# Performance work log

Hardware: AMD Instinct MI355X
Metric: run time of the kernel (lower is better)

Reference implementation:

```python
import jax, jax.numpy as jnp
import numpy as np

D = 512
H = 8
DV = D // H  # 64
NEG_INF = -1e30


def setup_inputs() -> dict:
    key = jax.random.key(0)
    ks = jax.random.split(key, 10)
    B, S = 4, 2048
    x = jax.random.normal(ks[0], (B, D, S), dtype=jnp.float32)
    mask = jnp.ones((B, S), dtype=jnp.float32)
    s = 1.0 / np.sqrt(D)
    sv = 1.0 / np.sqrt(D)
    # per-head Linear(d -> dv) weights stacked: [H, dv, d] (torch Linear layout W @ x)
    Wq = jax.random.uniform(ks[1], (H, DV, D), jnp.float32, -s, s)
    bq = jax.random.uniform(ks[2], (H, DV), jnp.float32, -s, s)
    Wk = jax.random.uniform(ks[3], (H, DV, D), jnp.float32, -s, s)
    bk = jax.random.uniform(ks[4], (H, DV), jnp.float32, -s, s)
    Wv = jax.random.uniform(ks[5], (H, DV, D), jnp.float32, -s, s)
    bv = jax.random.uniform(ks[6], (H, DV), jnp.float32, -s, s)
    W0 = jax.random.uniform(ks[7], (D, D), jnp.float32, -sv, sv)
    b0 = jax.random.uniform(ks[8], (D,), jnp.float32, -sv, sv)
    return {"x": x, "mask": mask, "Wq": Wq, "bq": bq, "Wk": Wk, "bk": bk,
            "Wv": Wv, "bv": bv, "W0": W0, "b0": b0}


def reference(x, mask, Wq, bq, Wk, bk, Wv, bv, W0, b0):
    # x: [B, d, S] -> xt: [B, S, d]
    xt = jnp.transpose(x, (0, 2, 1))
    # fused per-head projections: [B, H, S, dv]
    q = jnp.einsum('bsd,hed->bhse', xt, Wq) + bq[None, :, None, :]
    k = jnp.einsum('bsd,hed->bhse', xt, Wk) + bk[None, :, None, :]
    v = jnp.einsum('bsd,hed->bhse', xt, Wv) + bv[None, :, None, :]
    dv = q.shape[-1]
    scores = jnp.einsum('bhse,bhte->bhst', q, k) * (1.0 / np.sqrt(dv))
    # mask_logits (QANet style): keep where mask==1, else -1e30; mask over key dim
    h_mask = mask[:, None, None, :]  # [B,1,1,S]
    scores = scores * h_mask + (1.0 - h_mask) * NEG_INF
    p = jax.nn.softmax(scores, axis=-1)
    # zero out fully-masked query rows via v_mask on query dim
    p = p * mask[:, None, :, None]
    out = jnp.einsum('bhst,bhte->bhse', p, v)  # [B,H,S,dv]
    # concat heads along feature dim -> [B, S, d]
    B, _, S, _ = out.shape
    heads = jnp.transpose(out, (0, 2, 1, 3)).reshape(B, S, -1)
    y = heads @ W0.T + b0  # output projection
    return jnp.transpose(y, (0, 2, 1))  # [B, d, S]
```

## Files before the change

kernel.cpp:

```cpp
#include <hip/hip_runtime.h>

#define B_  4
#define D_  512
#define H_  8
#define DV_ 64
#define S_  2048
#define LOG2E 1.442695041f

typedef __bf16 bf16;
typedef bf16  bf16x8 __attribute__((ext_vector_type(8)));
typedef bf16  bf16x4 __attribute__((ext_vector_type(4)));
typedef float f32x4  __attribute__((ext_vector_type(4)));

#define MFMA(a, b, c) __builtin_amdgcn_mfma_f32_16x16x32_bf16((a), (b), (c), 0, 0, 0)

#define GLOAD_LDS(g, l)                                                     \
    __builtin_amdgcn_global_load_lds(                                       \
        (const __attribute__((address_space(1))) void*)(g),                 \
        (__attribute__((address_space(3))) void*)(l), 16, 0, 0)

__global__ __launch_bounds__(256) void prep(
    const float* __restrict__ x, const float* __restrict__ Wq,
    const float* __restrict__ Wk, const float* __restrict__ Wv,
    const float* __restrict__ W0, bf16* __restrict__ xb, bf16* __restrict__ Wb) {
    const int bid = blockIdx.x;
    if (bid < 4096) {
        __shared__ float tile[32][33];
        const int sblk = bid % 64;
        const int dblk = (bid / 64) % 16;
        const int b    = bid / 1024;
        const int d0 = dblk * 32, s0 = sblk * 32;
        const int tx = threadIdx.x & 31;
        const int ty = threadIdx.x >> 5;
        const float* xp = x + (size_t)b * D_ * S_;
#pragma unroll
        for (int i = 0; i < 32; i += 8)
            tile[ty + i][tx] = xp[(size_t)(d0 + ty + i) * S_ + s0 + tx];
        __syncthreads();
        bf16* xbp = xb + ((size_t)b * S_ + s0) * D_ + d0;
#pragma unroll
        for (int i = 0; i < 32; i += 8)
            xbp[(size_t)(ty + i) * D_ + tx] = (bf16)tile[tx][ty + i];
    } else {
        const int f0 = ((bid - 4096) * 256 + threadIdx.x) * 16;
        const int src = f0 >> 18;
        const int off = f0 & 262143;
        const float* W = (src == 0) ? Wq : (src == 1) ? Wk : (src == 2) ? Wv : W0;
        float4 v0 = *(const float4*)&W[off];
        float4 v1 = *(const float4*)&W[off + 4];
        float4 v2 = *(const float4*)&W[off + 8];
        float4 v3 = *(const float4*)&W[off + 12];
        bf16x8 h0 = {(bf16)v0.x, (bf16)v0.y, (bf16)v0.z, (bf16)v0.w,
                     (bf16)v1.x, (bf16)v1.y, (bf16)v1.z, (bf16)v1.w};
        bf16x8 h1 = {(bf16)v2.x, (bf16)v2.y, (bf16)v2.z, (bf16)v2.w,
                     (bf16)v3.x, (bf16)v3.y, (bf16)v3.z, (bf16)v3.w};
        *(bf16x8*)&Wb[f0]     = h0;
        *(bf16x8*)&Wb[f0 + 8] = h1;
    }
}

__global__ __launch_bounds__(256) void gemm_qkv(
    const bf16* __restrict__ A, const bf16* __restrict__ Wb,
    const float* __restrict__ bq, const float* __restrict__ bk,
    const float* __restrict__ bv,
    bf16* __restrict__ Q, bf16* __restrict__ K, bf16* __restrict__ Vt) {
    __shared__ union {
        struct { bf16 A[8192]; bf16 B[8192]; } s;
        bf16 T[128][132];
    } sm;

    const int tid = threadIdx.x;
    const int w = tid >> 6, lane = tid & 63;
    const int m16 = lane & 15, quad = lane >> 4;
    const int wr = w & 1, wc = w >> 1;

    const int nblk = blockIdx.x % 12;
    const int mblk = blockIdx.x / 12;
    const int m0 = mblk * 128, n0 = nblk * 128;

    f32x4 acc[4][4];
#pragma unroll
    for (int i = 0; i < 4; ++i)
#pragma unroll
        for (int j = 0; j < 4; ++j) acc[i][j] = (f32x4){0.f, 0.f, 0.f, 0.f};

    for (int k0 = 0; k0 < D_; k0 += 64) {
        __syncthreads();
#pragma unroll
        for (int i = 0; i < 4; ++i) {
            const int c  = w * 4 + i;
            const int mt = c >> 1, kk = c & 1;
            const int row = mt * 16 + m16;
            const int col = k0 + kk * 32 + quad * 8;
            GLOAD_LDS(&A[(size_t)(m0 + row) * D_ + col],  &sm.s.A[(c * 64 + lane) * 8]);
            GLOAD_LDS(&Wb[(size_t)(n0 + row) * D_ + col], &sm.s.B[(c * 64 + lane) * 8]);
        }
        __syncthreads();
#pragma unroll
        for (int kk = 0; kk < 2; ++kk) {
            bf16x8 af[4], bfv[4];
#pragma unroll
            for (int t = 0; t < 4; ++t) {
                af[t]  = *(const bf16x8*)&sm.s.A[(((wr * 4 + t) * 2 + kk) * 64 + lane) * 8];
                bfv[t] = *(const bf16x8*)&sm.s.B[(((wc * 4 + t) * 2 + kk) * 64 + lane) * 8];
            }
#pragma unroll
            for (int mt = 0; mt < 4; ++mt)
#pragma unroll
                for (int nt = 0; nt < 4; ++nt)
                    acc[mt][nt] = MFMA(af[mt], bfv[nt], acc[mt][nt]);
        }
    }

    const int proj = n0 >> 9;
    const float* bias = (proj == 0) ? bq : (proj == 1) ? bk : bv;

    if (proj == 2) {
#pragma unroll
        for (int mt = 0; mt < 4; ++mt)
#pragma unroll
            for (int nt = 0; nt < 4; ++nt) {
                const int nr = (n0 + wc * 64 + nt * 16 + m16) & 511;
                const int h = nr >> 6, e = nr & 63;
                const float bia = bias[nr];
                const int srow = m0 + wr * 64 + mt * 16 + quad * 4;
                const int b = srow >> 11, s = srow & 2047;
                const int s2 = (s & ~31) | (quad * 8 + (mt & 1) * 4);
                bf16x4 hv;
#pragma unroll
                for (int r = 0; r < 4; ++r) hv[r] = (bf16)(acc[mt][nt][r] + bia);
                *(bf16x4*)&Vt[(((size_t)b * H_ + h) * DV_ + e) * S_ + s2] = hv;
            }
    } else {
        __syncthreads();
#pragma unroll
        for (int mt = 0; mt < 4; ++mt)
#pragma unroll
            for (int nt = 0; nt < 4; ++nt) {
                const int nloc = wc * 64 + nt * 16 + m16;
                const float bia = bias[(n0 + nloc) & 511];
#pragma unroll
                for (int r = 0; r < 4; ++r)
                    sm.T[wr * 64 + mt * 16 + quad * 4 + r][nloc] =
                        (bf16)(acc[mt][nt][r] + bia);
            }
        __syncthreads();
        const int rloc = tid >> 1, cb = (tid & 1) * 64;
        const int M = m0 + rloc, b = M >> 11, s = M & 2047;
        const int nrb = (n0 + cb) & 511;
        const int h = nrb >> 6;
        bf16* dst = ((proj == 0) ? Q : K) + (((size_t)b * H_ + h) * S_ + s) * DV_;
#pragma unroll
        for (int u = 0; u < 8; ++u)
            *(bf16x8*)&dst[u * 8] = *(const bf16x8*)&sm.T[rloc][cb + u * 8];
    }
}

#define LOADK(DST, TW)                                                       \
    {                                                                        \
        _Pragma("unroll")                                                    \
        for (int tt = 0; tt < 2; ++tt)                                       \
            _Pragma("unroll")                                                \
            for (int kk = 0; kk < 2; ++kk)                                   \
                DST[tt][kk] = *(const bf16x8*)&Kp[                           \
                    (size_t)((TW) + tt * 16 + m16) * DV_ + kk * 32 + quad * 8]; \
    }

#define COMPUTE(TW, KF)                                                      \
    {                                                                        \
        const int tw_ = (TW);                                                \
        bf16x8 vfr[4];                                                       \
        _Pragma("unroll")                                                    \
        for (int mt = 0; mt < 4; ++mt)                                       \
            vfr[mt] = *(const bf16x8*)&Vp[(size_t)(mt * 16 + m16) * S_ +     \
                                          tw_ + quad * 8];                   \
        const f32x4 m2a = *(const f32x4*)&sm.Ms[tw_ + quad * 4];             \
        const f32x4 m2b = *(const f32x4*)&sm.Ms[tw_ + 16 + quad * 4];        \
        f32x4 sc[2][4];                                                      \
        _Pragma("unroll")                                                    \
        for (int tt = 0; tt < 2; ++tt)                                       \
            _Pragma("unroll")                                                \
            for (int qt = 0; qt < 4; ++qt)                                   \
                sc[tt][qt] = (f32x4){0.f, 0.f, 0.f, 0.f};                    \
        _Pragma("unroll")                                                    \
        for (int kk = 0; kk < 2; ++kk)                                       \
            _Pragma("unroll")                                                \
            for (int tt = 0; tt < 2; ++tt)                                   \
                _Pragma("unroll")                                            \
                for (int qt = 0; qt < 4; ++qt)                               \
                    sc[tt][qt] = MFMA(KF[tt][kk], qf[qt][kk], sc[tt][qt]);   \
        f32x4 ngA, ngB;                                                      \
        _Pragma("unroll")                                                    \
        for (int r = 0; r < 4; ++r) {                                        \
            ngA[r] = (m2a[r] - LOG2E) * 8e29f;                               \
            ngB[r] = (m2b[r] - LOG2E) * 8e29f;                               \
        }                                                                    \
        bf16x8 pf[4];                                                        \
        _Pragma("unroll")                                                    \
        for (int qt = 0; qt < 4; ++qt)                                       \
            _Pragma("unroll")                                                \
            for (int r = 0; r < 4; ++r) {                                    \
                pf[qt][r] = (bf16)__builtin_amdgcn_exp2f(                    \
                    __builtin_fmaf(sc[0][qt][r], m2a[r], ngA[r]));           \
                pf[qt][4 + r] = (bf16)__builtin_amdgcn_exp2f(                \
                    __builtin_fmaf(sc[1][qt][r], m2b[r], ngB[r]));           \
            }                                                                \
        _Pragma("unroll")                                                    \
        for (int mt = 0; mt < 4; ++mt)                                       \
            _Pragma("unroll")                                                \
            for (int qt = 0; qt < 4; ++qt)                                   \
                o[mt][qt] = MFMA(vfr[mt], pf[qt], o[mt][qt]);                \
        _Pragma("unroll")                                                    \
        for (int qt = 0; qt < 4; ++qt)                                       \
            lacc[qt] = MFMA(ones, pf[qt], lacc[qt]);                         \
    }

__global__ __launch_bounds__(256, 2) void flash_attn(
    const bf16* __restrict__ Q, const bf16* __restrict__ K, const bf16* __restrict__ Vt,
    const float* __restrict__ mask, bf16* __restrict__ heads) {
    __shared__ union {
        float Ms[2048];
        struct { float O[64][65]; float L[64]; } red;
    } sm;

    const int bid  = blockIdx.x;
    const int bidx = (bid & 7) * 128 + (bid >> 3);
    const int qblk = bidx & 31;
    const int h    = (bidx >> 5) & 7;
    const int b    = bidx >> 8;
    const int q0   = qblk * 64;

    const int tid = threadIdx.x;
    const int w = tid >> 6, lane = tid & 63;
    const int m16 = lane & 15, quad = lane >> 4;

    const bf16* Qp = Q  + ((size_t)b * H_ + h) * S_ * DV_;
    const bf16* Kp = K  + ((size_t)b * H_ + h) * S_ * DV_;
    const bf16* Vp = Vt + ((size_t)b * H_ + h) * DV_ * S_;
    const float* mp = mask + (size_t)b * S_;

#pragma unroll
    for (int p = 0; p < 2; ++p) {
        const float4 mv = *(const float4*)&mp[(p * 256 + tid) * 4];
        f32x4 t = {mv.x * LOG2E, mv.y * LOG2E, mv.z * LOG2E, mv.w * LOG2E};
        *(f32x4*)&sm.Ms[(p * 256 + tid) * 4] = t;
    }

    bf16x8 qf[4][2];
#pragma unroll
    for (int qt = 0; qt < 4; ++qt)
#pragma unroll
        for (int kk = 0; kk < 2; ++kk) {
            bf16x8 v = *(const bf16x8*)&Qp[(size_t)(q0 + qt * 16 + m16) * DV_ +
                                           kk * 32 + quad * 8];
#pragma unroll
            for (int i = 0; i < 8; ++i) v[i] = (bf16)((float)v[i] * 0.125f);
            qf[qt][kk] = v;
        }

    bf16x8 ones;
#pragma unroll
    for (int i = 0; i < 8; ++i) ones[i] = (bf16)1.0f;

    f32x4 o[4][4];
    f32x4 lacc[4];
#pragma unroll
    for (int mt = 0; mt < 4; ++mt)
#pragma unroll
        for (int qt = 0; qt < 4; ++qt) o[mt][qt] = (f32x4){0.f, 0.f, 0.f, 0.f};
#pragma unroll
    for (int qt = 0; qt < 4; ++qt) lacc[qt] = (f32x4){0.f, 0.f, 0.f, 0.f};

    bf16x8 kfA[2][2], kfB[2][2];
    LOADK(kfA, w * 32);
    __syncthreads();

    for (int i = 0; i < 16; i += 2) {
        LOADK(kfB, (i + 1) * 128 + w * 32);
        COMPUTE(i * 128 + w * 32, kfA);
        if (i < 14) LOADK(kfA, (i + 2) * 128 + w * 32);
        COMPUTE((i + 1) * 128 + w * 32, kfB);
    }

    __syncthreads();
#pragma unroll
    for (int ww = 0; ww < 4; ++ww) {
        if (w == ww) {
#pragma unroll
            for (int mt = 0; mt < 4; ++mt)
#pragma unroll
                for (int qt = 0; qt < 4; ++qt)
#pragma unroll
                    for (int r = 0; r < 4; ++r) {
                        float* slot = &sm.red.O[mt * 16 + quad * 4 + r][qt * 16 + m16];
                        *slot = (ww == 0) ? o[mt][qt][r] : (*slot + o[mt][qt][r]);
                    }
            if (quad == 0)
#pragma unroll
                for (int qt = 0; qt < 4; ++qt) {
                    float* ls = &sm.red.L[qt * 16 + m16];
                    *ls = (ww == 0) ? lacc[qt][0] : (*ls + lacc[qt][0]);
                }
        }
        __syncthreads();
    }

    const int ql = tid >> 2, ec = (tid & 3) * 16;
    const float l  = sm.red.L[ql];
    const float qm = mp[q0 + ql];
    const float inv = qm / l;
    bf16x8 hv[2];
#pragma unroll
    for (int c = 0; c < 2; ++c)
#pragma unroll
        for (int i = 0; i < 8; ++i)
            hv[c][i] = (bf16)(sm.red.O[ec + c * 8 + i][ql] * inv);
    bf16* dst = &heads[((size_t)b * S_ + q0 + ql) * D_ + h * DV_ + ec];
    *(bf16x8*)(dst)     = hv[0];
    *(bf16x8*)(dst + 8) = hv[1];
}

__global__ __launch_bounds__(256) void gemm_out(
    const bf16* __restrict__ A, const bf16* __restrict__ Wb,
    const float* __restrict__ b0, float* __restrict__ outp) {
    __shared__ bf16 Asl[8192];
    __shared__ bf16 Bsl[8192];

    const int tid = threadIdx.x;
    const int w = tid >> 6, lane = tid & 63;
    const int m16 = lane & 15, quad = lane >> 4;
    const int wr = w & 1, wc = w >> 1;

    const int nblk = blockIdx.x & 3;
    const int mblk = blockIdx.x >> 2;
    const int m0 = mblk * 128, n0 = nblk * 128;

    f32x4 acc[4][4];
#pragma unroll
    for (int i = 0; i < 4; ++i)
#pragma unroll
        for (int j = 0; j < 4; ++j) acc[i][j] = (f32x4){0.f, 0.f, 0.f, 0.f};

    for (int k0 = 0; k0 < D_; k0 += 64) {
        __syncthreads();
#pragma unroll
        for (int i = 0; i < 4; ++i) {
            const int c  = w * 4 + i;
            const int mt = c >> 1, kk = c & 1;
            const int row = mt * 16 + m16;
            const int col = k0 + kk * 32 + quad * 8;
            GLOAD_LDS(&A[(size_t)(m0 + row) * D_ + col], &Asl[(c * 64 + lane) * 8]);
            GLOAD_LDS(&Wb[(size_t)(1536 + n0 + row) * D_ + col], &Bsl[(c * 64 + lane) * 8]);
        }
        __syncthreads();
#pragma unroll
        for (int kk = 0; kk < 2; ++kk) {
            bf16x8 af[4], bfv[4];
#pragma unroll
            for (int t = 0; t < 4; ++t) {
                af[t]  = *(const bf16x8*)&Asl[(((wr * 4 + t) * 2 + kk) * 64 + lane) * 8];
                bfv[t] = *(const bf16x8*)&Bsl[(((wc * 4 + t) * 2 + kk) * 64 + lane) * 8];
            }
#pragma unroll
            for (int mt = 0; mt < 4; ++mt)
#pragma unroll
                for (int nt = 0; nt < 4; ++nt)
                    acc[mt][nt] = MFMA(af[mt], bfv[nt], acc[mt][nt]);
        }
    }

#pragma unroll
    for (int mt = 0; mt < 4; ++mt)
#pragma unroll
        for (int nt = 0; nt < 4; ++nt) {
            const int n = n0 + wc * 64 + nt * 16 + m16;
            const float bia = b0[n];
            const int srow = m0 + wr * 64 + mt * 16 + quad * 4;
            const int b = srow >> 11, s = srow & 2047;
            float4 vv;
            vv.x = acc[mt][nt][0] + bia;
            vv.y = acc[mt][nt][1] + bia;
            vv.z = acc[mt][nt][2] + bia;
            vv.w = acc[mt][nt][3] + bia;
            *(float4*)&outp[((size_t)b * D_ + n) * S_ + s] = vv;
        }
}

extern "C" void kernel_launch(void* const* d_in, const int* in_sizes, int n_in,
                              void* d_out, int out_size, void* d_ws, size_t ws_size,
                              hipStream_t stream) {
    const float* x    = (const float*)d_in[0];
    const float* mask = (const float*)d_in[1];
    const float* Wq   = (const float*)d_in[2];
    const float* bq   = (const float*)d_in[3];
    const float* Wk   = (const float*)d_in[4];
    const float* bk   = (const float*)d_in[5];
    const float* Wv   = (const float*)d_in[6];
    const float* bv   = (const float*)d_in[7];
    const float* W0   = (const float*)d_in[8];
    const float* b0   = (const float*)d_in[9];
    float* out = (float*)d_out;

    char* ws = (char*)d_ws;
    const size_t SEG = (size_t)B_ * S_ * D_ * sizeof(bf16);
    bf16* xb    = (bf16*)(ws);
    bf16* Qb    = (bf16*)(ws + SEG);
    bf16* Kb    = (bf16*)(ws + 2 * SEG);
    bf16* Vt    = (bf16*)(ws + 3 * SEG);
    bf16* Wb    = (bf16*)(ws + 4 * SEG);
    bf16* heads = xb;

    prep<<<dim3(4096 + 256), dim3(256), 0, stream>>>(x, Wq, Wk, Wv, W0, xb, Wb);
    gemm_qkv<<<dim3(64 * 12), dim3(256), 0, stream>>>(xb, Wb, bq, bk, bv, Qb, Kb, Vt);
    flash_attn<<<dim3(B_ * H_ * (S_ / 64)), dim3(256), 0, stream>>>(Qb, Kb, Vt, mask, heads);
    gemm_out<<<dim3(64 * 4), dim3(256), 0, stream>>>(heads, Wb, b0, out);
}
```

Before: 210.0 us.

## Restructure flash attention to share LDS-staged K/V tiles and remap GEMM blocks

The attention kernel changes from each wave owning a slice of keys for all 64 queries (followed by a cross-wave LDS reduction of O) to each wave owning 16 queries and iterating over all keys. K and V tiles are double-buffered in swizzled LDS through async global-to-LDS loads, so they are fetched once per block instead of each wave reading its own slice from global. This removes the serial four-step reduction and cuts per-wave register use enough to raise occupancy to 3 blocks per CU. The cost is a barrier per 64-key tile. Both GEMMs also remap block indices so that consecutive blocks are spread across XCDs for better cache locality.

```diff
diff --git a/kernel.cpp b/kernel.cpp
--- a/kernel.cpp
+++ b/kernel.cpp
@@ -74,8 +74,9 @@
     const int m16 = lane & 15, quad = lane >> 4;
     const int wr = w & 1, wc = w >> 1;
 
-    const int nblk = blockIdx.x % 12;
-    const int mblk = blockIdx.x / 12;
+    const int bid  = (blockIdx.x & 7) * 96 + (blockIdx.x >> 3);
+    const int nblk = bid % 12;
+    const int mblk = bid / 12;
     const int m0 = mblk * 128, n0 = nblk * 128;
 
     f32x4 acc[4][4];
@@ -156,71 +157,16 @@
     }
 }
 
-#define LOADK(DST, TW)                                                       \
-    {                                                                        \
-        _Pragma("unroll")                                                    \
-        for (int tt = 0; tt < 2; ++tt)                                       \
-            _Pragma("unroll")                                                \
-            for (int kk = 0; kk < 2; ++kk)                                   \
-                DST[tt][kk] = *(const bf16x8*)&Kp[                           \
-                    (size_t)((TW) + tt * 16 + m16) * DV_ + kk * 32 + quad * 8]; \
-    }
-
-#define COMPUTE(TW, KF)                                                      \
-    {                                                                        \
-        const int tw_ = (TW);                                                \
-        bf16x8 vfr[4];                                                       \
-        _Pragma("unroll")                                                    \
-        for (int mt = 0; mt < 4; ++mt)                                       \
-            vfr[mt] = *(const bf16x8*)&Vp[(size_t)(mt * 16 + m16) * S_ +     \
-                                          tw_ + quad * 8];                   \
-        const f32x4 m2a = *(const f32x4*)&sm.Ms[tw_ + quad * 4];             \
-        const f32x4 m2b = *(const f32x4*)&sm.Ms[tw_ + 16 + quad * 4];        \
-        f32x4 sc[2][4];                                                      \
-        _Pragma("unroll")                                                    \
-        for (int tt = 0; tt < 2; ++tt)                                       \
-            _Pragma("unroll")                                                \
-            for (int qt = 0; qt < 4; ++qt)                                   \
-                sc[tt][qt] = (f32x4){0.f, 0.f, 0.f, 0.f};                    \
-        _Pragma("unroll")                                                    \
-        for (int kk = 0; kk < 2; ++kk)                                       \
-            _Pragma("unroll")                                                \
-            for (int tt = 0; tt < 2; ++tt)                                   \
-                _Pragma("unroll")                                            \
-                for (int qt = 0; qt < 4; ++qt)                               \
-                    sc[tt][qt] = MFMA(KF[tt][kk], qf[qt][kk], sc[tt][qt]);   \
-        f32x4 ngA, ngB;                                                      \
-        _Pragma("unroll")                                                    \
-        for (int r = 0; r < 4; ++r) {                                        \
-            ngA[r] = (m2a[r] - LOG2E) * 8e29f;                               \
-            ngB[r] = (m2b[r] - LOG2E) * 8e29f;                               \
-        }                                                                    \
-        bf16x8 pf[4];                                                        \
-        _Pragma("unroll")                                                    \
-        for (int qt = 0; qt < 4; ++qt)                                       \
-            _Pragma("unroll")                                                \
-            for (int r = 0; r < 4; ++r) {                                    \
-                pf[qt][r] = (bf16)__builtin_amdgcn_exp2f(                    \
-                    __builtin_fmaf(sc[0][qt][r], m2a[r], ngA[r]));           \
-                pf[qt][4 + r] = (bf16)__builtin_amdgcn_exp2f(                \
-                    __builtin_fmaf(sc[1][qt][r], m2b[r], ngB[r]));           \
-            }                                                                \
-        _Pragma("unroll")                                                    \
-        for (int mt = 0; mt < 4; ++mt)                                       \
-            _Pragma("unroll")                                                \
-            for (int qt = 0; qt < 4; ++qt)                                   \
-                o[mt][qt] = MFMA(vfr[mt], pf[qt], o[mt][qt]);                \
-        _Pragma("unroll")                                                    \
-        for (int qt = 0; qt < 4; ++qt)                                       \
-            lacc[qt] = MFMA(ones, pf[qt], lacc[qt]);                         \
-    }
-
-__global__ __launch_bounds__(256, 2) void flash_attn(
+__global__ __launch_bounds__(256, 3) void flash_attn(
     const bf16* __restrict__ Q, const bf16* __restrict__ K, const bf16* __restrict__ Vt,
     const float* __restrict__ mask, bf16* __restrict__ heads) {
     __shared__ union {
-        float Ms[2048];
-        struct { float O[64][65]; float L[64]; } red;
+        struct {
+            bf16 Kl[2][2][2048];
+            bf16 Vl[2][2][2048];
+            float Ms[2048];
+        } s;
+        bf16 ep[4][16][72];
     } sm;
 
     const int bid  = blockIdx.x;
@@ -239,85 +185,122 @@
     const bf16* Vp = Vt + ((size_t)b * H_ + h) * DV_ * S_;
     const float* mp = mask + (size_t)b * S_;
 
+    const int krow = lane >> 3;
+    const int kcol = ((lane & 7) ^ krow) * 8;
+    const int vrow = lane >> 2;
+    const int vcol = ((lane & 3) ^ (vrow & 3)) * 8;
+    const int sh  = w >> 1;
+    const int sp0 = (w & 1) * 2;
+
+#define STAGE(NB, T0)                                                        \
+    {                                                                        \
+        _Pragma("unroll")                                                    \
+        for (int j = 0; j < 2; ++j) {                                        \
+            const int p = sp0 + j;                                           \
+            GLOAD_LDS(&Kp[(size_t)((T0) + sh * 32 + p * 8 + krow) * DV_ + kcol], \
+                      &sm.s.Kl[NB][sh][(p * 64 + lane) * 8]);                \
+        }                                                                    \
+        _Pragma("unroll")                                                    \
+        for (int j = 0; j < 2; ++j) {                                        \
+            const int p = sp0 + j;                                           \
+            GLOAD_LDS(&Vp[(size_t)(p * 16 + vrow) * S_ + (T0) + sh * 32 + vcol], \
+                      &sm.s.Vl[NB][sh][(p * 64 + lane) * 8]);                \
+        }                                                                    \
+    }
+
 #pragma unroll
     for (int p = 0; p < 2; ++p) {
         const float4 mv = *(const float4*)&mp[(p * 256 + tid) * 4];
         f32x4 t = {mv.x * LOG2E, mv.y * LOG2E, mv.z * LOG2E, mv.w * LOG2E};
-        *(f32x4*)&sm.Ms[(p * 256 + tid) * 4] = t;
-    }
-
-    bf16x8 qf[4][2];
-#pragma unroll
-    for (int qt = 0; qt < 4; ++qt)
-#pragma unroll
-        for (int kk = 0; kk < 2; ++kk) {
-            bf16x8 v = *(const bf16x8*)&Qp[(size_t)(q0 + qt * 16 + m16) * DV_ +
-                                           kk * 32 + quad * 8];
-#pragma unroll
-            for (int i = 0; i < 8; ++i) v[i] = (bf16)((float)v[i] * 0.125f);
-            qf[qt][kk] = v;
-        }
+        *(f32x4*)&sm.s.Ms[(p * 256 + tid) * 4] = t;
+    }
+
+    bf16x8 qf[2];
+#pragma unroll
+    for (int kk = 0; kk < 2; ++kk) {
+        bf16x8 v = *(const bf16x8*)&Qp[(size_t)(q0 + w * 16 + m16) * DV_ +
+                                       kk * 32 + quad * 8];
+#pragma unroll
+        for (int i = 0; i < 8; ++i) v[i] = (bf16)((float)v[i] * 0.125f);
+        qf[kk] = v;
+    }
 
     bf16x8 ones;
 #pragma unroll
     for (int i = 0; i < 8; ++i) ones[i] = (bf16)1.0f;
 
-    f32x4 o[4][4];
-    f32x4 lacc[4];
-#pragma unroll
-    for (int mt = 0; mt < 4; ++mt)
-#pragma unroll
-        for (int qt = 0; qt < 4; ++qt) o[mt][qt] = (f32x4){0.f, 0.f, 0.f, 0.f};
-#pragma unroll
-    for (int qt = 0; qt < 4; ++qt) lacc[qt] = (f32x4){0.f, 0.f, 0.f, 0.f};
-
-    bf16x8 kfA[2][2], kfB[2][2];
-    LOADK(kfA, w * 32);
+    f32x4 o[4];
+    f32x4 lacc = (f32x4){0.f, 0.f, 0.f, 0.f};
+#pragma unroll
+    for (int mt = 0; mt < 4; ++mt) o[mt] = (f32x4){0.f, 0.f, 0.f, 0.f};
+
+    STAGE(0, 0);
     __syncthreads();
 
-    for (int i = 0; i < 16; i += 2) {
-        LOADK(kfB, (i + 1) * 128 + w * 32);
-        COMPUTE(i * 128 + w * 32, kfA);
-        if (i < 14) LOADK(kfA, (i + 2) * 128 + w * 32);
-        COMPUTE((i + 1) * 128 + w * 32, kfB);
-    }
-
-    __syncthreads();
-#pragma unroll
-    for (int ww = 0; ww < 4; ++ww) {
-        if (w == ww) {
-#pragma unroll
-            for (int mt = 0; mt < 4; ++mt)
-#pragma unroll
-                for (int qt = 0; qt < 4; ++qt)
-#pragma unroll
-                    for (int r = 0; r < 4; ++r) {
-                        float* slot = &sm.red.O[mt * 16 + quad * 4 + r][qt * 16 + m16];
-                        *slot = (ww == 0) ? o[mt][qt][r] : (*slot + o[mt][qt][r]);
-                    }
-            if (quad == 0)
-#pragma unroll
-                for (int qt = 0; qt < 4; ++qt) {
-                    float* ls = &sm.red.L[qt * 16 + m16];
-                    *ls = (ww == 0) ? lacc[qt][0] : (*ls + lacc[qt][0]);
+    for (int i = 0; i < 32; ++i) {
+        const int buf = i & 1;
+        if (i < 31) STAGE(buf ^ 1, (i + 1) * 64);
+        const int t0 = i * 64;
+
+        f32x4 sc[4];
+#pragma unroll
+        for (int kt = 0; kt < 4; ++kt) sc[kt] = (f32x4){0.f, 0.f, 0.f, 0.f};
+#pragma unroll
+        for (int kh = 0; kh < 2; ++kh)
+#pragma unroll
+            for (int tt = 0; tt < 2; ++tt)
+#pragma unroll
+                for (int kk = 0; kk < 2; ++kk) {
+                    const bf16x8 kf = *(const bf16x8*)&sm.s.Kl[buf][kh][
+                        ((tt * 16 + m16) * 8 + ((kk * 4 + quad) ^ (m16 & 7))) * 8];
+                    sc[kh * 2 + tt] = MFMA(kf, qf[kk], sc[kh * 2 + tt]);
                 }
-        }
-        __syncthreads();
-    }
-
-    const int ql = tid >> 2, ec = (tid & 3) * 16;
-    const float l  = sm.red.L[ql];
-    const float qm = mp[q0 + ql];
-    const float inv = qm / l;
-    bf16x8 hv[2];
-#pragma unroll
-    for (int c = 0; c < 2; ++c)
-#pragma unroll
-        for (int i = 0; i < 8; ++i)
-            hv[c][i] = (bf16)(sm.red.O[ec + c * 8 + i][ql] * inv);
-    bf16* dst = &heads[((size_t)b * S_ + q0 + ql) * D_ + h * DV_ + ec];
-    *(bf16x8*)(dst)     = hv[0];
-    *(bf16x8*)(dst + 8) = hv[1];
+
+        bf16x8 pf[2];
+#pragma unroll
+        for (int kh = 0; kh < 2; ++kh) {
+            const f32x4 m2a = *(const f32x4*)&sm.s.Ms[t0 + kh * 32 + quad * 4];
+            const f32x4 m2b = *(const f32x4*)&sm.s.Ms[t0 + kh * 32 + 16 + quad * 4];
+#pragma unroll
+            for (int r = 0; r < 4; ++r) {
+                const float ngA = (m2a[r] - LOG2E) * 8e29f;
+                const float ngB = (m2b[r] - LOG2E) * 8e29f;
+                pf[kh][r]     = (bf16)__builtin_amdgcn_exp2f(
+                    __builtin_fmaf(sc[kh * 2 + 0][r], m2a[r], ngA));
+                pf[kh][4 + r] = (bf16)__builtin_amdgcn_exp2f(
+                    __builtin_fmaf(sc[kh * 2 + 1][r], m2b[r], ngB));
+            }
+        }
+#pragma unroll
+        for (int kh = 0; kh < 2; ++kh) lacc = MFMA(ones, pf[kh], lacc);
+#pragma unroll
+        for (int kh = 0; kh < 2; ++kh)
+#pragma unroll
+            for (int mt = 0; mt < 4; ++mt) {
+                const bf16x8 vf = *(const bf16x8*)&sm.s.Vl[buf][kh][
+                    ((mt * 16 + m16) * 4 + (quad ^ (m16 & 3))) * 8];
+                o[mt] = MFMA(vf, pf[kh], o[mt]);
+            }
+
+        __syncthreads();
+    }
+
+    const float qm = mp[q0 + w * 16 + m16];
+    const float inv = qm / lacc[0];
+#pragma unroll
+    for (int mt = 0; mt < 4; ++mt) {
+        bf16x4 hv;
+#pragma unroll
+        for (int r = 0; r < 4; ++r) hv[r] = (bf16)(o[mt][r] * inv);
+        *(bf16x4*)&sm.ep[w][m16][mt * 16 + quad * 4] = hv;
+    }
+    const int ql = lane >> 2, ec = (lane & 3) * 16;
+    const bf16x8 h0 = *(const bf16x8*)&sm.ep[w][ql][ec];
+    const bf16x8 h1 = *(const bf16x8*)&sm.ep[w][ql][ec + 8];
+    bf16* dst = &heads[((size_t)b * S_ + q0 + w * 16 + ql) * D_ + h * DV_ + ec];
+    *(bf16x8*)(dst)     = h0;
+    *(bf16x8*)(dst + 8) = h1;
+#undef STAGE
 }
 
 __global__ __launch_bounds__(256) void gemm_out(
@@ -331,8 +314,9 @@
     const int m16 = lane & 15, quad = lane >> 4;
     const int wr = w & 1, wc = w >> 1;
 
-    const int nblk = blockIdx.x & 3;
-    const int mblk = blockIdx.x >> 2;
+    const int bid  = (blockIdx.x & 7) * 32 + (blockIdx.x >> 3);
+    const int nblk = bid & 3;
+    const int mblk = bid >> 2;
     const int m0 = mblk * 128, n0 = nblk * 128;
 
     f32x4 acc[4][4];
```

After: 269.5 us. 28.3% more time.
